# Performance work log

Hardware: AMD Instinct MI355X
Metric: run time of the kernel (lower is better)

The kernel has to match this reference:

```python
import jax, jax.numpy as jnp
import numpy as np

EPS = 1e-08


def setup_inputs() -> dict:
    key = jax.random.key(0)
    ks = jax.random.split(key, 9)
    B, T, H, W = 128, 32, 32, 32
    Z = 128
    d = {}
    d['x_seq'] = jax.random.normal(ks[0], (B, T, H, W), dtype=jnp.float32)
    # encoder MLP: 1024 -> 256 -> 128 (kaiming-ish scale)
    d['We1'] = jax.random.normal(ks[1], (H * W, 256), dtype=jnp.float32) * (2.0 / (H * W)) ** 0.5
    d['be1'] = jnp.zeros((256,), jnp.float32)
    d['We2'] = jax.random.normal(ks[2], (256, Z), dtype=jnp.float32) * (2.0 / 256) ** 0.5
    d['be2'] = jnp.zeros((Z,), jnp.float32)
    # context norm params
    d['gamma'] = jnp.ones((Z,), jnp.float32)
    d['beta'] = jnp.zeros((Z,), jnp.float32)
    # g_theta: (128+1)*2=258 -> 512 -> 256
    d['Wg1'] = jax.random.normal(ks[3], (258, 512), dtype=jnp.float32) * (2.0 / 258) ** 0.5
    d['bg1'] = jnp.zeros((512,), jnp.float32)
    d['Wg2'] = jax.random.normal(ks[4], (512, 256), dtype=jnp.float32) * (2.0 / 512) ** 0.5
    d['bg2'] = jnp.zeros((256,), jnp.float32)
    # f_phi: 256 -> 256 -> y_dim=4
    d['Wf'] = jax.random.normal(ks[5], (256, 256), dtype=jnp.float32) * (2.0 / 256) ** 0.5
    d['bf'] = jnp.zeros((256,), jnp.float32)
    d['Wy'] = jax.random.normal(ks[6], (256, 4), dtype=jnp.float32) * (1.0 / 256) ** 0.5
    d['by'] = jnp.zeros((4,), jnp.float32)
    return d


def reference(x_seq, We1, be1, We2, be2, gamma, beta, Wg1, bg1, Wg2, bg2, Wf, bf, Wy, by):
    B, T, H, W = x_seq.shape
    # Encoder (MLP stand-in), vectorized over the sequence dim
    x = x_seq.reshape(B, T, H * W)
    h = jax.nn.relu(jnp.einsum('btd,dk->btk', x, We1) + be1)
    z = jnp.einsum('btk,kz->btz', h, We2) + be2          # [B,T,128]
    # Context norm over the sequence dim (torch .var() is unbiased, ddof=1)
    mu = z.mean(axis=1, keepdims=True)
    sigma = jnp.sqrt(z.var(axis=1, keepdims=True, ddof=1) + EPS)
    z = (z - mu) / sigma * gamma + beta
    # Append temporal tag
    tag = jnp.broadcast_to(jnp.arange(T, dtype=z.dtype)[None, :, None], (B, T, 1))
    z = jnp.concatenate([z, tag], axis=2)                # [B,T,129]
    # Relation network over all T^2 ordered pairs, batched as one GEMM.
    # g_hidden = relu([z_i, z_j] @ Wg1 + bg1); split Wg1 to avoid materializing the concat.
    Wg1_a, Wg1_b = Wg1[:129], Wg1[129:]
    gi = jnp.einsum('bic,ch->bih', z, Wg1_a)             # [B,T,512]
    gj = jnp.einsum('bjc,ch->bjh', z, Wg1_b)             # [B,T,512]
    g_hidden = jax.nn.relu(gi[:, :, None, :] + gj[:, None, :, :] + bg1)  # [B,T,T,512]
    g_out = jax.nn.relu(jnp.einsum('bijh,hg->bijg', g_hidden, Wg2) + bg2)
    all_g = g_out.sum(axis=(1, 2))                       # [B,256]
    f_hidden = jax.nn.relu(all_g @ Wf + bf)
    y_pred_linear = f_hidden @ Wy + by                   # [B,4]
    y_pred = jnp.argmax(y_pred_linear, axis=1)
    return (y_pred_linear, y_pred)
```

## Files before the change

kernel.cpp:

```cpp
#include <hip/hip_runtime.h>
#include <hip/hip_bf16.h>

#define EPS 1e-8f

typedef __attribute__((ext_vector_type(8))) short short8;
typedef __attribute__((ext_vector_type(4))) float f32x4;

__device__ __forceinline__ unsigned short f2bf(float f) {
  union { float f; unsigned u; } v; v.f = f;
  unsigned r = v.u + 0x7fffu + ((v.u >> 16) & 1u);
  return (unsigned short)(r >> 16);
}
__device__ __forceinline__ float bf2f(unsigned short b) {
  union { unsigned u; float f; } v; v.u = ((unsigned)b) << 16;
  return v.f;
}
__device__ __forceinline__ unsigned pack_bf2(float lo, float hi) {
  unsigned r;
  asm("v_cvt_pk_bf16_f32 %0, %1, %2" : "=v"(r) : "v"(lo), "v"(hi));
  return r;
}

__global__ __launch_bounds__(256) void k0_prep(const float* __restrict__ We1,
                                               const float* __restrict__ We2,
                                               const float* __restrict__ Wg1,
                                               const float* __restrict__ Wg2,
                                               const float* __restrict__ Wf,
                                               unsigned short* __restrict__ We1T,
                                               unsigned short* __restrict__ We2T,
                                               unsigned short* __restrict__ Wg1T,
                                               unsigned short* __restrict__ Wg2T,
                                               unsigned short* __restrict__ WfT) {
  int idx = blockIdx.x * 256 + threadIdx.x;
  if (idx < 262144) {
    int n = idx >> 10, k = idx & 1023;
    We1T[idx] = f2bf(We1[k * 256 + n]);
  } else if (idx < 294912) {
    int e = idx - 262144;
    int n = e >> 8, k = e & 255;
    We2T[e] = f2bf(We2[k * 128 + n]);
  } else if (idx < 458752) {
    int e = idx - 294912;
    int n = e / 160, c = e % 160;
    float v = 0.f;
    if (c < 129) v = (n < 512) ? Wg1[c * 512 + n] : Wg1[(129 + c) * 512 + (n - 512)];
    Wg1T[e] = f2bf(v);
  } else if (idx < 589824) {
    int e = idx - 458752;
    int n = e >> 9, k = e & 511;
    Wg2T[e] = f2bf(Wg2[k * 256 + n]);
  } else {
    int e = idx - 589824;
    int n = e >> 8, k = e & 255;
    WfT[e] = f2bf(Wf[k * 256 + n]);
  }
}

__global__ __launch_bounds__(512, 2) void k1(const float* __restrict__ x,
                                             const unsigned short* __restrict__ We1T,
                                             const float* __restrict__ be1,
                                             unsigned short* __restrict__ h_bf) {
  __shared__ unsigned char As[2][8192];
  int tid = threadIdx.x, lane = tid & 63, w = tid >> 6;
  int m0 = blockIdx.x * 16;
  int srow = tid >> 5, skk = (tid & 31) * 8;
  int cb = w * 32;
  int row = lane & 15, kg = (lane >> 4) * 8;

  f32x4 acc[2] = {{0,0,0,0},{0,0,0,0}};

  auto stage = [&](int kc, int buf) {
    const float* src = x + (size_t)(m0 + srow) * 1024 + kc * 256 + skk;
    float4 a = *reinterpret_cast<const float4*>(src);
    float4 b = *reinterpret_cast<const float4*>(src + 4);
    uint4 pv;
    pv.x = pack_bf2(a.x, a.y); pv.y = pack_bf2(a.z, a.w);
    pv.z = pack_bf2(b.x, b.y); pv.w = pack_bf2(b.z, b.w);
    int addr = (srow * 512 + skk * 2) ^ ((srow & 7) << 4);
    *reinterpret_cast<uint4*>(&As[buf][addr]) = pv;
  };

  stage(0, 0);
  __syncthreads();
  for (int kc = 0; kc < 4; ++kc) {
    if (kc < 3) stage(kc + 1, (kc + 1) & 1);
    short8 breg[2][8];
#pragma unroll
    for (int cf = 0; cf < 2; ++cf)
#pragma unroll
      for (int ks = 0; ks < 8; ++ks)
        breg[cf][ks] = *reinterpret_cast<const short8*>(
            We1T + (size_t)(cb + cf * 16 + row) * 1024 + kc * 256 + ks * 32 + kg);
    const unsigned char* hc = &As[kc & 1][0];
#pragma unroll
    for (int ks = 0; ks < 8; ++ks) {
      int aoff = (row * 512 + ks * 64 + kg * 2) ^ ((row & 7) << 4);
      short8 af = *reinterpret_cast<const short8*>(hc + aoff);
      acc[0] = __builtin_amdgcn_mfma_f32_16x16x32_bf16(af, breg[0][ks], acc[0], 0, 0, 0);
      acc[1] = __builtin_amdgcn_mfma_f32_16x16x32_bf16(af, breg[1][ks], acc[1], 0, 0, 0);
    }
    __syncthreads();
  }
#pragma unroll
  for (int cf = 0; cf < 2; ++cf) {
    int col = cb + cf * 16 + row;
    float bias = be1[col];
#pragma unroll
    for (int r = 0; r < 4; ++r) {
      int orow = m0 + (lane >> 4) * 4 + r;
      h_bf[(size_t)orow * 256 + col] = f2bf(fmaxf(acc[cf][r] + bias, 0.f));
    }
  }
}

__global__ __launch_bounds__(256) void k2a(const unsigned short* __restrict__ h_bf,
                                           const unsigned short* __restrict__ We2T,
                                           const float* __restrict__ be2,
                                           const float* __restrict__ gamma,
                                           const float* __restrict__ beta,
                                           unsigned short* __restrict__ zc) {
  __shared__ unsigned char zcs[16384];
  __shared__ float zb[32][132];
  int b = blockIdx.x, tid = threadIdx.x, lane = tid & 63, w = tid >> 6;
  int row = lane & 15, kg = (lane >> 4) * 8;

  {
    int srow = tid >> 3, skk = (tid & 7) * 32;
#pragma unroll
    for (int q = 0; q < 4; ++q) {
      short8 v = *reinterpret_cast<const short8*>(
          h_bf + (size_t)(b * 32 + srow) * 256 + skk + q * 8);
      int addr = (srow * 512 + (skk + q * 8) * 2) ^ ((srow & 7) << 4);
      *reinterpret_cast<short8*>(&zcs[addr]) = v;
    }
  }
  short8 breg1[2][8];
#pragma unroll
  for (int cf = 0; cf < 2; ++cf)
#pragma unroll
    for (int ks = 0; ks < 8; ++ks)
      breg1[cf][ks] = *reinterpret_cast<const short8*>(
          We2T + (size_t)(w * 32 + cf * 16 + row) * 256 + ks * 32 + kg);
  __syncthreads();

  {
    f32x4 acc[2][2] = {{{0,0,0,0},{0,0,0,0}},{{0,0,0,0},{0,0,0,0}}};
#pragma unroll
    for (int ks = 0; ks < 8; ++ks) {
      int a0off = (row * 512 + ks * 64 + kg * 2) ^ ((row & 7) << 4);
      int a1off = ((16 + row) * 512 + ks * 64 + kg * 2) ^ ((row & 7) << 4);
      short8 a0 = *reinterpret_cast<const short8*>(&zcs[a0off]);
      short8 a1 = *reinterpret_cast<const short8*>(&zcs[a1off]);
#pragma unroll
      for (int cf = 0; cf < 2; ++cf) {
        acc[0][cf] = __builtin_amdgcn_mfma_f32_16x16x32_bf16(a0, breg1[cf][ks], acc[0][cf], 0, 0, 0);
        acc[1][cf] = __builtin_amdgcn_mfma_f32_16x16x32_bf16(a1, breg1[cf][ks], acc[1][cf], 0, 0, 0);
      }
    }
#pragma unroll
    for (int rf = 0; rf < 2; ++rf)
#pragma unroll
      for (int cf = 0; cf < 2; ++cf) {
        int col = w * 32 + cf * 16 + row;
        float bias = be2[col];
#pragma unroll
        for (int r = 0; r < 4; ++r)
          zb[rf * 16 + (lane >> 4) * 4 + r][col] = acc[rf][cf][r] + bias;
      }
  }
  __syncthreads();

  if (tid < 128) {
    float s = 0.f, s2 = 0.f;
#pragma unroll 4
    for (int t = 0; t < 32; ++t) { float v = zb[t][tid]; s += v; s2 += v * v; }
    float mu = s * (1.f / 32.f);
    float var = (s2 - 32.f * mu * mu) * (1.f / 31.f);
    float rs = 1.f / sqrtf(fmaxf(var, 0.f) + EPS);
    float g = gamma[tid], be = beta[tid];
#pragma unroll 4
    for (int t = 0; t < 32; ++t)
      zc[(size_t)(b * 32 + t) * 160 + tid] = f2bf((zb[t][tid] - mu) * rs * g + be);
  } else if (tid < 160) {
    for (int t = 0; t < 32; ++t)
      zc[(size_t)(b * 32 + t) * 160 + tid] = (tid == 128) ? f2bf((float)t) : 0;
  }
}

__global__ __launch_bounds__(512, 4) void k2b(const unsigned short* __restrict__ zc,
                                              const unsigned short* __restrict__ Wg1T,
                                              const float* __restrict__ bg1,
                                              unsigned short* __restrict__ g_all) {
  __shared__ unsigned char As[16384];
  int m0 = (blockIdx.x >> 2) * 32;
  int n0 = (blockIdx.x & 3) * 256;
  int tid = threadIdx.x, lane = tid & 63, w = tid >> 6;
  int row = lane & 15, kg = (lane >> 4) * 8;
  int c0 = n0 + w * 32;

  for (int ch = tid; ch < 640; ch += 512) {
    int r = ch / 20, c16 = ch % 20;
    short8 v = *reinterpret_cast<const short8*>(zc + (size_t)(m0 + r) * 160 + c16 * 8);
    int addr = (r * 512 + c16 * 16) ^ ((r & 7) << 4);
    *reinterpret_cast<short8*>(&As[addr]) = v;
  }
  short8 breg[2][5];
#pragma unroll
  for (int cf = 0; cf < 2; ++cf)
#pragma unroll
    for (int ks = 0; ks < 5; ++ks)
      breg[cf][ks] = *reinterpret_cast<const short8*>(
          Wg1T + (size_t)(c0 + cf * 16 + row) * 160 + ks * 32 + kg);
  __syncthreads();

  f32x4 acc[2][2] = {{{0,0,0,0},{0,0,0,0}},{{0,0,0,0},{0,0,0,0}}};
#pragma unroll
  for (int ks = 0; ks < 5; ++ks) {
    int a0off = (row * 512 + ks * 64 + kg * 2) ^ ((row & 7) << 4);
    int a1off = ((16 + row) * 512 + ks * 64 + kg * 2) ^ ((row & 7) << 4);
    short8 a0 = *reinterpret_cast<const short8*>(&As[a0off]);
    short8 a1 = *reinterpret_cast<const short8*>(&As[a1off]);
#pragma unroll
    for (int cf = 0; cf < 2; ++cf) {
      acc[0][cf] = __builtin_amdgcn_mfma_f32_16x16x32_bf16(a0, breg[cf][ks], acc[0][cf], 0, 0, 0);
      acc[1][cf] = __builtin_amdgcn_mfma_f32_16x16x32_bf16(a1, breg[cf][ks], acc[1][cf], 0, 0, 0);
    }
  }
#pragma unroll
  for (int cf = 0; cf < 2; ++cf) {
    int n = c0 + cf * 16 + row;
    float bias = (n < 512) ? bg1[n] : 0.f;
#pragma unroll
    for (int rf = 0; rf < 2; ++rf)
#pragma unroll
      for (int r = 0; r < 4; ++r) {
        int mrow = m0 + rf * 16 + (lane >> 4) * 4 + r;
        g_all[((size_t)mrow << 10) + n] = f2bf(acc[rf][cf][r] + bias);
      }
  }
}

__global__ __launch_bounds__(512, 2) void k3(const unsigned short* __restrict__ g_all,
                                             const unsigned short* __restrict__ Wg2T,
                                             const float* __restrict__ bg2,
                                             float* __restrict__ all_gp) {
  __shared__ unsigned char ldsH[2][32768];
  int b = blockIdx.x >> 1, hi = blockIdx.x & 1;
  int ii0 = hi * 16;
  int tid = threadIdx.x, lane = tid & 63, w = tid >> 6;
  int row = lane & 15, kg16 = (lane >> 4) * 16;
  int cb = w * 32;
  int p = tid >> 4, kslot = tid & 15;

  short8 breg[2][16];
#pragma unroll
  for (int cf = 0; cf < 2; ++cf)
#pragma unroll
    for (int ks = 0; ks < 16; ++ks)
      breg[cf][ks] = *reinterpret_cast<const short8*>(
          Wg2T + (size_t)(cb + cf * 16 + row) * 512 + ks * 32 + (lane >> 4) * 8);

  float gjf[32];
  {
    const unsigned short* gjp = g_all + ((size_t)(b * 32 + p) << 10) + 512 + kslot * 8;
#pragma unroll
    for (int q = 0; q < 4; ++q) {
      short8 gv = *reinterpret_cast<const short8*>(gjp + q * 128);
#pragma unroll
      for (int e = 0; e < 8; ++e) gjf[q * 8 + e] = bf2f((unsigned short)gv[e]);
    }
  }
  float biasv[2] = { bg2[cb + row], bg2[cb + 16 + row] };
  float accsum[2] = { 0.f, 0.f };

  short8 gv[4];
  auto hload = [&](int ii) {
    const unsigned short* gi = g_all + ((size_t)(b * 32 + ii) << 10) + kslot * 8;
#pragma unroll
    for (int q = 0; q < 4; ++q)
      gv[q] = *reinterpret_cast<const short8*>(gi + q * 128);
  };
  auto hstore = [&](int buf) {
    unsigned char* hb = &ldsH[buf][0] + p * 1024;
#pragma unroll
    for (int q = 0; q < 4; ++q) {
      uint4 pv;
      float f0 = fmaxf(bf2f((unsigned short)gv[q][0]) + gjf[q * 8 + 0], 0.f);
      float f1 = fmaxf(bf2f((unsigned short)gv[q][1]) + gjf[q * 8 + 1], 0.f);
      float f2 = fmaxf(bf2f((unsigned short)gv[q][2]) + gjf[q * 8 + 2], 0.f);
      float f3 = fmaxf(bf2f((unsigned short)gv[q][3]) + gjf[q * 8 + 3], 0.f);
      float f4 = fmaxf(bf2f((unsigned short)gv[q][4]) + gjf[q * 8 + 4], 0.f);
      float f5 = fmaxf(bf2f((unsigned short)gv[q][5]) + gjf[q * 8 + 5], 0.f);
      float f6 = fmaxf(bf2f((unsigned short)gv[q][6]) + gjf[q * 8 + 6], 0.f);
      float f7 = fmaxf(bf2f((unsigned short)gv[q][7]) + gjf[q * 8 + 7], 0.f);
      pv.x = pack_bf2(f0, f1); pv.y = pack_bf2(f2, f3);
      pv.z = pack_bf2(f4, f5); pv.w = pack_bf2(f6, f7);
      int addr = (kslot * 16 + q * 256) ^ ((p & 7) << 4);
      *reinterpret_cast<uint4*>(hb + addr) = pv;
    }
  };

  hload(ii0);
  hstore(0);
  __syncthreads();

  for (int it = 0; it < 16; ++it) {
    if (it < 15) hload(ii0 + it + 1);
    const unsigned char* hc = &ldsH[it & 1][0];
    f32x4 acc[2][2] = {{{0,0,0,0},{0,0,0,0}},{{0,0,0,0},{0,0,0,0}}};
    short8 a0 = *reinterpret_cast<const short8*>(hc + ((row * 1024 + kg16) ^ ((row & 7) << 4)));
    short8 a1 = *reinterpret_cast<const short8*>(hc + (((16 + row) * 1024 + kg16) ^ ((row & 7) << 4)));
#pragma unroll
    for (int ks = 0; ks < 16; ++ks) {
      short8 c0v = a0, c1v = a1;
      if (ks < 15) {
        a0 = *reinterpret_cast<const short8*>(hc + ((row * 1024 + (ks + 1) * 64 + kg16) ^ ((row & 7) << 4)));
        a1 = *reinterpret_cast<const short8*>(hc + (((16 + row) * 1024 + (ks + 1) * 64 + kg16) ^ ((row & 7) << 4)));
      }
      __builtin_amdgcn_s_setprio(1);
      acc[0][0] = __builtin_amdgcn_mfma_f32_16x16x32_bf16(c0v, breg[0][ks], acc[0][0], 0, 0, 0);
      acc[0][1] = __builtin_amdgcn_mfma_f32_16x16x32_bf16(c0v, breg[1][ks], acc[0][1], 0, 0, 0);
      acc[1][0] = __builtin_amdgcn_mfma_f32_16x16x32_bf16(c1v, breg[0][ks], acc[1][0], 0, 0, 0);
      acc[1][1] = __builtin_amdgcn_mfma_f32_16x16x32_bf16(c1v, breg[1][ks], acc[1][1], 0, 0, 0);
      __builtin_amdgcn_s_setprio(0);
    }
    if (it < 15) hstore((it + 1) & 1);
#pragma unroll
    for (int cf = 0; cf < 2; ++cf)
#pragma unroll
      for (int rf = 0; rf < 2; ++rf)
#pragma unroll
        for (int r = 0; r < 4; ++r)
          accsum[cf] += fmaxf(acc[rf][cf][r] + biasv[cf], 0.f);
    __syncthreads();
  }

#pragma unroll
  for (int cf = 0; cf < 2; ++cf) {
    accsum[cf] += __shfl_xor(accsum[cf], 16, 64);
    accsum[cf] += __shfl_xor(accsum[cf], 32, 64);
  }
  if ((lane >> 4) == 0) {
#pragma unroll
    for (int cf = 0; cf < 2; ++cf)
      all_gp[(size_t)(hi * 128 + b) * 256 + cb + cf * 16 + lane] = accsum[cf];
  }
}

__global__ __launch_bounds__(512) void k4(const float* __restrict__ all_gp,
                                          const unsigned short* __restrict__ WfT,
                                          const float* __restrict__ bfv,
                                          const float* __restrict__ Wy,
                                          const float* __restrict__ by,
                                          float* __restrict__ out) {
  __shared__ unsigned char As[8192];
  __shared__ float fh[16][264];
  __shared__ float wys[1024];
  __shared__ float yvs[16][4];
  int tid = threadIdx.x, lane = tid & 63, w = tid >> 6;
  int row = lane & 15, kg = (lane >> 4) * 8;
  int m0 = blockIdx.x * 16;

  {
    int r = tid >> 5, c8 = (tid & 31) * 8;
    const float* p0 = all_gp + (size_t)(m0 + r) * 256 + c8;
    const float* p1 = all_gp + (size_t)(128 + m0 + r) * 256 + c8;
    float4 a0 = *reinterpret_cast<const float4*>(p0);
    float4 a1 = *reinterpret_cast<const float4*>(p0 + 4);
    float4 b0 = *reinterpret_cast<const float4*>(p1);
    float4 b1 = *reinterpret_cast<const float4*>(p1 + 4);
    uint4 pv;
    pv.x = pack_bf2(a0.x + b0.x, a0.y + b0.y);
    pv.y = pack_bf2(a0.z + b0.z, a0.w + b0.w);
    pv.z = pack_bf2(a1.x + b1.x, a1.y + b1.y);
    pv.w = pack_bf2(a1.z + b1.z, a1.w + b1.w);
    int addr = (r * 512 + c8 * 2) ^ ((r & 7) << 4);
    *reinterpret_cast<uint4*>(&As[addr]) = pv;
  }
  wys[tid] = Wy[tid];
  wys[tid + 512] = Wy[tid + 512];
  short8 breg[2][8];
#pragma unroll
  for (int cf = 0; cf < 2; ++cf)
#pragma unroll
    for (int ks = 0; ks < 8; ++ks)
      breg[cf][ks] = *reinterpret_cast<const short8*>(
          WfT + (size_t)(w * 32 + cf * 16 + row) * 256 + ks * 32 + kg);
  __syncthreads();

  f32x4 acc[2] = {{0,0,0,0},{0,0,0,0}};
#pragma unroll
  for (int ks = 0; ks < 8; ++ks) {
    int aoff = (row * 512 + ks * 64 + kg * 2) ^ ((row & 7) << 4);
    short8 af = *reinterpret_cast<const short8*>(&As[aoff]);
    acc[0] = __builtin_amdgcn_mfma_f32_16x16x32_bf16(af, breg[0][ks], acc[0], 0, 0, 0);
    acc[1] = __builtin_amdgcn_mfma_f32_16x16x32_bf16(af, breg[1][ks], acc[1], 0, 0, 0);
  }
#pragma unroll
  for (int cf = 0; cf < 2; ++cf) {
    int col = w * 32 + cf * 16 + row;
    float bias = bfv[col];
#pragma unroll
    for (int r = 0; r < 4; ++r)
      fh[(lane >> 4) * 4 + r][col] = fmaxf(acc[cf][r] + bias, 0.f);
  }
  __syncthreads();

  if (tid < 64) {
    int r = tid >> 2, o = tid & 3;
    float y = by[o];
#pragma unroll 4
    for (int k = 0; k < 256; ++k) y += fh[r][k] * wys[k * 4 + o];
    yvs[r][o] = y;
    out[(m0 + r) * 4 + o] = y;
  }
  __syncthreads();
  if (tid < 16) {
    int am = 0;
    float best = yvs[tid][0];
#pragma unroll
    for (int o = 1; o < 4; ++o)
      if (yvs[tid][o] > best) { best = yvs[tid][o]; am = o; }
    out[512 + m0 + tid] = (float)am;
  }
}

extern "C" void kernel_launch(void* const* d_in, const int* in_sizes, int n_in,
                              void* d_out, int out_size, void* d_ws, size_t ws_size,
                              hipStream_t stream) {
  const float* x     = (const float*)d_in[0];
  const float* We1   = (const float*)d_in[1];
  const float* be1   = (const float*)d_in[2];
  const float* We2   = (const float*)d_in[3];
  const float* be2   = (const float*)d_in[4];
  const float* gamma = (const float*)d_in[5];
  const float* beta  = (const float*)d_in[6];
  const float* Wg1   = (const float*)d_in[7];
  const float* bg1   = (const float*)d_in[8];
  const float* Wg2   = (const float*)d_in[9];
  const float* bg2   = (const float*)d_in[10];
  const float* Wf    = (const float*)d_in[11];
  const float* bff   = (const float*)d_in[12];
  const float* Wy    = (const float*)d_in[13];
  const float* by    = (const float*)d_in[14];

  char* ws = (char*)d_ws;
  unsigned short* h_bf  = (unsigned short*)(ws + 0);
  unsigned short* g_all = (unsigned short*)(ws + 2097152);
  unsigned short* We1T  = (unsigned short*)(ws + 10485760);
  unsigned short* We2T  = (unsigned short*)(ws + 11010048);
  unsigned short* Wg1T  = (unsigned short*)(ws + 11075584);
  unsigned short* Wg2T  = (unsigned short*)(ws + 11403264);
  float*          all_gp= (float*)(ws + 11665408);
  unsigned short* WfT   = (unsigned short*)(ws + 11927552);
  unsigned short* zc    = (unsigned short*)(ws + 12058624);
  float*          out   = (float*)d_out;

  k0_prep<<<2560, 256, 0, stream>>>(We1, We2, Wg1, Wg2, Wf, We1T, We2T, Wg1T, Wg2T, WfT);
  k1<<<256, 512, 0, stream>>>(x, We1T, be1, h_bf);
  k2a<<<128, 256, 0, stream>>>(h_bf, We2T, be2, gamma, beta, zc);
  k2b<<<512, 512, 0, stream>>>(zc, Wg1T, bg1, g_all);
  k3<<<256, 512, 0, stream>>>(g_all, Wg2T, bg2, all_gp);
  k4<<<8, 512, 0, stream>>>(all_gp, WfT, bff, Wy, by, out);
}
```

Before: 84.02 us.

## Fuse context-norm with Wg1 projection and switch pair GEMM to 32x32 MFMA

Merges k2a and k2b into a single kernel. The normalized z tile stays in shared memory and is multiplied directly by Wg1, which drops the zc round trip through global memory and one launch. The cost is that each of the four column-quarter blocks per batch recomputes the We2 projection and the normalization. Separately, k3's pair GEMM now uses 32x32x16 bf16 MFMA with one 16-float accumulator per wave instead of four 16x16x32 tiles, which changes the register and LDS read pattern.

```diff
diff --git a/kernel.cpp b/kernel.cpp
--- a/kernel.cpp
+++ b/kernel.cpp
@@ -5,6 +5,7 @@
 
 typedef __attribute__((ext_vector_type(8))) short short8;
 typedef __attribute__((ext_vector_type(4))) float f32x4;
+typedef __attribute__((ext_vector_type(16))) float f32x16;
 
 __device__ __forceinline__ unsigned short f2bf(float f) {
   union { float f; unsigned u; } v; v.f = f;
@@ -113,15 +114,18 @@
   }
 }
 
-__global__ __launch_bounds__(256) void k2a(const unsigned short* __restrict__ h_bf,
-                                           const unsigned short* __restrict__ We2T,
-                                           const float* __restrict__ be2,
-                                           const float* __restrict__ gamma,
-                                           const float* __restrict__ beta,
-                                           unsigned short* __restrict__ zc) {
+__global__ __launch_bounds__(256) void k2(const unsigned short* __restrict__ h_bf,
+                                          const unsigned short* __restrict__ We2T,
+                                          const float* __restrict__ be2,
+                                          const float* __restrict__ gamma,
+                                          const float* __restrict__ beta,
+                                          const unsigned short* __restrict__ Wg1T,
+                                          const float* __restrict__ bg1,
+                                          unsigned short* __restrict__ g_all) {
   __shared__ unsigned char zcs[16384];
   __shared__ float zb[32][132];
-  int b = blockIdx.x, tid = threadIdx.x, lane = tid & 63, w = tid >> 6;
+  int b = blockIdx.x >> 2, nq = blockIdx.x & 3;
+  int tid = threadIdx.x, lane = tid & 63, w = tid >> 6;
   int row = lane & 15, kg = (lane >> 4) * 8;
 
   {
@@ -179,64 +183,58 @@
     float rs = 1.f / sqrtf(fmaxf(var, 0.f) + EPS);
     float g = gamma[tid], be = beta[tid];
 #pragma unroll 4
-    for (int t = 0; t < 32; ++t)
-      zc[(size_t)(b * 32 + t) * 160 + tid] = f2bf((zb[t][tid] - mu) * rs * g + be);
+    for (int t = 0; t < 32; ++t) {
+      unsigned short v = f2bf((zb[t][tid] - mu) * rs * g + be);
+      int addr = (t * 512 + tid * 2) ^ ((t & 7) << 4);
+      *reinterpret_cast<unsigned short*>(&zcs[addr]) = v;
+    }
   } else if (tid < 160) {
-    for (int t = 0; t < 32; ++t)
-      zc[(size_t)(b * 32 + t) * 160 + tid] = (tid == 128) ? f2bf((float)t) : 0;
-  }
-}
-
-__global__ __launch_bounds__(512, 4) void k2b(const unsigned short* __restrict__ zc,
-                                              const unsigned short* __restrict__ Wg1T,
-                                              const float* __restrict__ bg1,
-                                              unsigned short* __restrict__ g_all) {
-  __shared__ unsigned char As[16384];
-  int m0 = (blockIdx.x >> 2) * 32;
-  int n0 = (blockIdx.x & 3) * 256;
-  int tid = threadIdx.x, lane = tid & 63, w = tid >> 6;
-  int row = lane & 15, kg = (lane >> 4) * 8;
-  int c0 = n0 + w * 32;
-
-  for (int ch = tid; ch < 640; ch += 512) {
-    int r = ch / 20, c16 = ch % 20;
-    short8 v = *reinterpret_cast<const short8*>(zc + (size_t)(m0 + r) * 160 + c16 * 8);
-    int addr = (r * 512 + c16 * 16) ^ ((r & 7) << 4);
-    *reinterpret_cast<short8*>(&As[addr]) = v;
-  }
-  short8 breg[2][5];
-#pragma unroll
-  for (int cf = 0; cf < 2; ++cf)
+    for (int t = 0; t < 32; ++t) {
+      unsigned short v = (tid == 128) ? f2bf((float)t) : 0;
+      int addr = (t * 512 + tid * 2) ^ ((t & 7) << 4);
+      *reinterpret_cast<unsigned short*>(&zcs[addr]) = v;
+    }
+  }
+  __syncthreads();
+
+  {
+    int n0 = nq * 256 + w * 64;
+    short8 af[2][5];
+#pragma unroll
+    for (int rf = 0; rf < 2; ++rf)
+#pragma unroll
+      for (int ks = 0; ks < 5; ++ks) {
+        int aoff = ((rf * 16 + row) * 512 + ks * 64 + kg * 2) ^ ((row & 7) << 4);
+        af[rf][ks] = *reinterpret_cast<const short8*>(&zcs[aoff]);
+      }
+    short8 breg[4][5];
+#pragma unroll
+    for (int cf = 0; cf < 4; ++cf)
+#pragma unroll
+      for (int ks = 0; ks < 5; ++ks)
+        breg[cf][ks] = *reinterpret_cast<const short8*>(
+            Wg1T + (size_t)(n0 + cf * 16 + row) * 160 + ks * 32 + kg);
+    f32x4 acc[2][4] = {{{0,0,0,0},{0,0,0,0},{0,0,0,0},{0,0,0,0}},
+                       {{0,0,0,0},{0,0,0,0},{0,0,0,0},{0,0,0,0}}};
 #pragma unroll
     for (int ks = 0; ks < 5; ++ks)
-      breg[cf][ks] = *reinterpret_cast<const short8*>(
-          Wg1T + (size_t)(c0 + cf * 16 + row) * 160 + ks * 32 + kg);
-  __syncthreads();
-
-  f32x4 acc[2][2] = {{{0,0,0,0},{0,0,0,0}},{{0,0,0,0},{0,0,0,0}}};
-#pragma unroll
-  for (int ks = 0; ks < 5; ++ks) {
-    int a0off = (row * 512 + ks * 64 + kg * 2) ^ ((row & 7) << 4);
-    int a1off = ((16 + row) * 512 + ks * 64 + kg * 2) ^ ((row & 7) << 4);
-    short8 a0 = *reinterpret_cast<const short8*>(&As[a0off]);
-    short8 a1 = *reinterpret_cast<const short8*>(&As[a1off]);
-#pragma unroll
-    for (int cf = 0; cf < 2; ++cf) {
-      acc[0][cf] = __builtin_amdgcn_mfma_f32_16x16x32_bf16(a0, breg[cf][ks], acc[0][cf], 0, 0, 0);
-      acc[1][cf] = __builtin_amdgcn_mfma_f32_16x16x32_bf16(a1, breg[cf][ks], acc[1][cf], 0, 0, 0);
-    }
-  }
-#pragma unroll
-  for (int cf = 0; cf < 2; ++cf) {
-    int n = c0 + cf * 16 + row;
-    float bias = (n < 512) ? bg1[n] : 0.f;
-#pragma unroll
-    for (int rf = 0; rf < 2; ++rf)
-#pragma unroll
-      for (int r = 0; r < 4; ++r) {
-        int mrow = m0 + rf * 16 + (lane >> 4) * 4 + r;
-        g_all[((size_t)mrow << 10) + n] = f2bf(acc[rf][cf][r] + bias);
+#pragma unroll
+      for (int cf = 0; cf < 4; ++cf) {
+        acc[0][cf] = __builtin_amdgcn_mfma_f32_16x16x32_bf16(af[0][ks], breg[cf][ks], acc[0][cf], 0, 0, 0);
+        acc[1][cf] = __builtin_amdgcn_mfma_f32_16x16x32_bf16(af[1][ks], breg[cf][ks], acc[1][cf], 0, 0, 0);
       }
+#pragma unroll
+    for (int cf = 0; cf < 4; ++cf) {
+      int n = n0 + cf * 16 + row;
+      float bias = (n < 512) ? bg1[n] : 0.f;
+#pragma unroll
+      for (int rf = 0; rf < 2; ++rf)
+#pragma unroll
+        for (int r = 0; r < 4; ++r) {
+          int t = rf * 16 + (lane >> 4) * 4 + r;
+          g_all[((size_t)(b * 32 + t) << 10) + n] = f2bf(acc[rf][cf][r] + bias);
+        }
+    }
   }
 }
 
@@ -248,30 +246,28 @@
   int b = blockIdx.x >> 1, hi = blockIdx.x & 1;
   int ii0 = hi * 16;
   int tid = threadIdx.x, lane = tid & 63, w = tid >> 6;
-  int row = lane & 15, kg16 = (lane >> 4) * 16;
+  int l31 = lane & 31, lhi = lane >> 5;
   int cb = w * 32;
   int p = tid >> 4, kslot = tid & 15;
 
-  short8 breg[2][16];
-#pragma unroll
-  for (int cf = 0; cf < 2; ++cf)
-#pragma unroll
-    for (int ks = 0; ks < 16; ++ks)
-      breg[cf][ks] = *reinterpret_cast<const short8*>(
-          Wg2T + (size_t)(cb + cf * 16 + row) * 512 + ks * 32 + (lane >> 4) * 8);
+  short8 breg[32];
+#pragma unroll
+  for (int s = 0; s < 32; ++s)
+    breg[s] = *reinterpret_cast<const short8*>(
+        Wg2T + (size_t)(cb + l31) * 512 + s * 16 + lhi * 8);
 
   float gjf[32];
   {
     const unsigned short* gjp = g_all + ((size_t)(b * 32 + p) << 10) + 512 + kslot * 8;
 #pragma unroll
     for (int q = 0; q < 4; ++q) {
-      short8 gv = *reinterpret_cast<const short8*>(gjp + q * 128);
-#pragma unroll
-      for (int e = 0; e < 8; ++e) gjf[q * 8 + e] = bf2f((unsigned short)gv[e]);
-    }
-  }
-  float biasv[2] = { bg2[cb + row], bg2[cb + 16 + row] };
-  float accsum[2] = { 0.f, 0.f };
+      short8 gv0 = *reinterpret_cast<const short8*>(gjp + q * 128);
+#pragma unroll
+      for (int e = 0; e < 8; ++e) gjf[q * 8 + e] = bf2f((unsigned short)gv0[e]);
+    }
+  }
+  float bias = bg2[cb + l31];
+  float accsum = 0.f;
 
   short8 gv[4];
   auto hload = [&](int ii) {
@@ -307,44 +303,32 @@
   for (int it = 0; it < 16; ++it) {
     if (it < 15) hload(ii0 + it + 1);
     const unsigned char* hc = &ldsH[it & 1][0];
-    f32x4 acc[2][2] = {{{0,0,0,0},{0,0,0,0}},{{0,0,0,0},{0,0,0,0}}};
-    short8 a0 = *reinterpret_cast<const short8*>(hc + ((row * 1024 + kg16) ^ ((row & 7) << 4)));
-    short8 a1 = *reinterpret_cast<const short8*>(hc + (((16 + row) * 1024 + kg16) ^ ((row & 7) << 4)));
-#pragma unroll
-    for (int ks = 0; ks < 16; ++ks) {
-      short8 c0v = a0, c1v = a1;
-      if (ks < 15) {
-        a0 = *reinterpret_cast<const short8*>(hc + ((row * 1024 + (ks + 1) * 64 + kg16) ^ ((row & 7) << 4)));
-        a1 = *reinterpret_cast<const short8*>(hc + (((16 + row) * 1024 + (ks + 1) * 64 + kg16) ^ ((row & 7) << 4)));
-      }
+    f32x16 acc = {0.f,0.f,0.f,0.f,0.f,0.f,0.f,0.f,0.f,0.f,0.f,0.f,0.f,0.f,0.f,0.f};
+    short8 ar[4];
+#pragma unroll
+    for (int s = 0; s < 4; ++s)
+      ar[s] = *reinterpret_cast<const short8*>(
+          hc + ((l31 * 1024 + s * 32 + lhi * 16) ^ ((l31 & 7) << 4)));
+#pragma unroll
+    for (int s = 0; s < 32; ++s) {
+      short8 cur = ar[s & 3];
+      if (s < 28)
+        ar[s & 3] = *reinterpret_cast<const short8*>(
+            hc + ((l31 * 1024 + (s + 4) * 32 + lhi * 16) ^ ((l31 & 7) << 4)));
       __builtin_amdgcn_s_setprio(1);
-      acc[0][0] = __builtin_amdgcn_mfma_f32_16x16x32_bf16(c0v, breg[0][ks], acc[0][0], 0, 0, 0);
-      acc[0][1] = __builtin_amdgcn_mfma_f32_16x16x32_bf16(c0v, breg[1][ks], acc[0][1], 0, 0, 0);
-      acc[1][0] = __builtin_amdgcn_mfma_f32_16x16x32_bf16(c1v, breg[0][ks], acc[1][0], 0, 0, 0);
-      acc[1][1] = __builtin_amdgcn_mfma_f32_16x16x32_bf16(c1v, breg[1][ks], acc[1][1], 0, 0, 0);
+      acc = __builtin_amdgcn_mfma_f32_32x32x16_bf16(cur, breg[s], acc, 0, 0, 0);
       __builtin_amdgcn_s_setprio(0);
     }
     if (it < 15) hstore((it + 1) & 1);
 #pragma unroll
-    for (int cf = 0; cf < 2; ++cf)
-#pragma unroll
-      for (int rf = 0; rf < 2; ++rf)
-#pragma unroll
-        for (int r = 0; r < 4; ++r)
-          accsum[cf] += fmaxf(acc[rf][cf][r] + biasv[cf], 0.f);
+    for (int r = 0; r < 16; ++r)
+      accsum += fmaxf(acc[r] + bias, 0.f);
     __syncthreads();
   }
 
-#pragma unroll
-  for (int cf = 0; cf < 2; ++cf) {
-    accsum[cf] += __shfl_xor(accsum[cf], 16, 64);
-    accsum[cf] += __shfl_xor(accsum[cf], 32, 64);
-  }
-  if ((lane >> 4) == 0) {
-#pragma unroll
-    for (int cf = 0; cf < 2; ++cf)
-      all_gp[(size_t)(hi * 128 + b) * 256 + cb + cf * 16 + lane] = accsum[cf];
-  }
+  accsum += __shfl_xor(accsum, 32, 64);
+  if (lane < 32)
+    all_gp[(size_t)(hi * 128 + b) * 256 + cb + l31] = accsum;
 }
 
 __global__ __launch_bounds__(512) void k4(const float* __restrict__ all_gp,
@@ -453,13 +437,11 @@
   unsigned short* Wg2T  = (unsigned short*)(ws + 11403264);
   float*          all_gp= (float*)(ws + 11665408);
   unsigned short* WfT   = (unsigned short*)(ws + 11927552);
-  unsigned short* zc    = (unsigned short*)(ws + 12058624);
   float*          out   = (float*)d_out;
 
   k0_prep<<<2560, 256, 0, stream>>>(We1, We2, Wg1, Wg2, Wf, We1T, We2T, Wg1T, Wg2T, WfT);
   k1<<<256, 512, 0, stream>>>(x, We1T, be1, h_bf);
-  k2a<<<128, 256, 0, stream>>>(h_bf, We2T, be2, gamma, beta, zc);
-  k2b<<<512, 512, 0, stream>>>(zc, Wg1T, bg1, g_all);
+  k2<<<512, 256, 0, stream>>>(h_bf, We2T, be2, gamma, beta, Wg1T, bg1, g_all);
   k3<<<256, 512, 0, stream>>>(g_all, Wg2T, bg2, all_gp);
   k4<<<8, 512, 0, stream>>>(all_gp, WfT, bff, Wy, by, out);
 }
```

After: 88.62 us. +5.5%, slower.

## Fuse encoder GEMMs with context norm and tile weight transposes through LDS

Applied to the files above, without the earlier changes.

Merges the first encoder GEMM (k1) with the second GEMM and context-norm kernel (k2a) into one per-batch kernel, k1f. The ReLU hidden activations stay in LDS instead of round-tripping through global memory, and one launch goes away. The weight-prep kernel now transposes 32x32 tiles through shared memory, so both global reads and writes are coalesced instead of strided. The cost is that the fused GEMM runs on 128 blocks instead of 256, which lowers parallelism on the first GEMM. Waves 4-7 also compute unused columns in the second GEMM: their We2T reads fall past the end of the We2T buffer and the results are discarded by the col<128 guard.

```diff
diff --git a/kernel.cpp b/kernel.cpp
--- a/kernel.cpp
+++ b/kernel.cpp
@@ -31,109 +31,143 @@
                                                unsigned short* __restrict__ Wg1T,
                                                unsigned short* __restrict__ Wg2T,
                                                unsigned short* __restrict__ WfT) {
-  int idx = blockIdx.x * 256 + threadIdx.x;
-  if (idx < 262144) {
-    int n = idx >> 10, k = idx & 1023;
-    We1T[idx] = f2bf(We1[k * 256 + n]);
-  } else if (idx < 294912) {
-    int e = idx - 262144;
-    int n = e >> 8, k = e & 255;
-    We2T[e] = f2bf(We2[k * 128 + n]);
-  } else if (idx < 458752) {
-    int e = idx - 294912;
-    int n = e / 160, c = e % 160;
-    float v = 0.f;
-    if (c < 129) v = (n < 512) ? Wg1[c * 512 + n] : Wg1[(129 + c) * 512 + (n - 512)];
-    Wg1T[e] = f2bf(v);
-  } else if (idx < 589824) {
-    int e = idx - 458752;
-    int n = e >> 9, k = e & 511;
-    Wg2T[e] = f2bf(Wg2[k * 256 + n]);
+  __shared__ float ld[32][33];
+  int t = blockIdx.x, tid = threadIdx.x;
+  int r0 = tid >> 5, c = tid & 31;
+
+  if (t < 256) {
+    int rb = (t >> 3) * 32, cb = (t & 7) * 32;
+#pragma unroll
+    for (int j = 0; j < 4; ++j)
+      ld[r0 + j * 8][c] = We1[(size_t)(rb + r0 + j * 8) * 256 + cb + c];
+    __syncthreads();
+#pragma unroll
+    for (int j = 0; j < 4; ++j)
+      We1T[(size_t)(cb + r0 + j * 8) * 1024 + rb + c] = f2bf(ld[c][r0 + j * 8]);
+  } else if (t < 288) {
+    int u = t - 256;
+    int rb = (u >> 2) * 32, cb = (u & 3) * 32;
+#pragma unroll
+    for (int j = 0; j < 4; ++j)
+      ld[r0 + j * 8][c] = We2[(size_t)(rb + r0 + j * 8) * 128 + cb + c];
+    __syncthreads();
+#pragma unroll
+    for (int j = 0; j < 4; ++j)
+      We2T[(size_t)(cb + r0 + j * 8) * 256 + rb + c] = f2bf(ld[c][r0 + j * 8]);
+  } else if (t < 416) {
+    int u = t - 288;
+    int rb = (u >> 3) * 32, cb = (u & 7) * 32;
+#pragma unroll
+    for (int j = 0; j < 4; ++j)
+      ld[r0 + j * 8][c] = Wg2[(size_t)(rb + r0 + j * 8) * 256 + cb + c];
+    __syncthreads();
+#pragma unroll
+    for (int j = 0; j < 4; ++j)
+      Wg2T[(size_t)(cb + r0 + j * 8) * 512 + rb + c] = f2bf(ld[c][r0 + j * 8]);
+  } else if (t < 480) {
+    int u = t - 416;
+    int rb = (u >> 3) * 32, cb = (u & 7) * 32;
+#pragma unroll
+    for (int j = 0; j < 4; ++j)
+      ld[r0 + j * 8][c] = Wf[(size_t)(rb + r0 + j * 8) * 256 + cb + c];
+    __syncthreads();
+#pragma unroll
+    for (int j = 0; j < 4; ++j)
+      WfT[(size_t)(cb + r0 + j * 8) * 256 + rb + c] = f2bf(ld[c][r0 + j * 8]);
   } else {
-    int e = idx - 589824;
-    int n = e >> 8, k = e & 255;
-    WfT[e] = f2bf(Wf[k * 256 + n]);
-  }
-}
-
-__global__ __launch_bounds__(512, 2) void k1(const float* __restrict__ x,
-                                             const unsigned short* __restrict__ We1T,
-                                             const float* __restrict__ be1,
-                                             unsigned short* __restrict__ h_bf) {
-  __shared__ unsigned char As[2][8192];
-  int tid = threadIdx.x, lane = tid & 63, w = tid >> 6;
-  int m0 = blockIdx.x * 16;
-  int srow = tid >> 5, skk = (tid & 31) * 8;
-  int cb = w * 32;
-  int row = lane & 15, kg = (lane >> 4) * 8;
-
-  f32x4 acc[2] = {{0,0,0,0},{0,0,0,0}};
-
-  auto stage = [&](int kc, int buf) {
-    const float* src = x + (size_t)(m0 + srow) * 1024 + kc * 256 + skk;
-    float4 a = *reinterpret_cast<const float4*>(src);
-    float4 b = *reinterpret_cast<const float4*>(src + 4);
-    uint4 pv;
-    pv.x = pack_bf2(a.x, a.y); pv.y = pack_bf2(a.z, a.w);
-    pv.z = pack_bf2(b.x, b.y); pv.w = pack_bf2(b.z, b.w);
-    int addr = (srow * 512 + skk * 2) ^ ((srow & 7) << 4);
-    *reinterpret_cast<uint4*>(&As[buf][addr]) = pv;
-  };
-
-  stage(0, 0);
-  __syncthreads();
-  for (int kc = 0; kc < 4; ++kc) {
-    if (kc < 3) stage(kc + 1, (kc + 1) & 1);
-    short8 breg[2][8];
-#pragma unroll
-    for (int cf = 0; cf < 2; ++cf)
-#pragma unroll
-      for (int ks = 0; ks < 8; ++ks)
-        breg[cf][ks] = *reinterpret_cast<const short8*>(
-            We1T + (size_t)(cb + cf * 16 + row) * 1024 + kc * 256 + ks * 32 + kg);
-    const unsigned char* hc = &As[kc & 1][0];
-#pragma unroll
-    for (int ks = 0; ks < 8; ++ks) {
-      int aoff = (row * 512 + ks * 64 + kg * 2) ^ ((row & 7) << 4);
-      short8 af = *reinterpret_cast<const short8*>(hc + aoff);
-      acc[0] = __builtin_amdgcn_mfma_f32_16x16x32_bf16(af, breg[0][ks], acc[0], 0, 0, 0);
-      acc[1] = __builtin_amdgcn_mfma_f32_16x16x32_bf16(af, breg[1][ks], acc[1], 0, 0, 0);
-    }
-    __syncthreads();
-  }
-#pragma unroll
-  for (int cf = 0; cf < 2; ++cf) {
-    int col = cb + cf * 16 + row;
-    float bias = be1[col];
-#pragma unroll
-    for (int r = 0; r < 4; ++r) {
-      int orow = m0 + (lane >> 4) * 4 + r;
-      h_bf[(size_t)orow * 256 + col] = f2bf(fmaxf(acc[cf][r] + bias, 0.f));
-    }
-  }
-}
-
-__global__ __launch_bounds__(256) void k2a(const unsigned short* __restrict__ h_bf,
+    int u = t - 480;
+    int nb = (u / 5) * 32, cb5 = (u % 5) * 32;
+#pragma unroll
+    for (int j = 0; j < 4; ++j) {
+      int cloc = r0 + j * 8, cidx = cb5 + cloc, n = nb + c;
+      float v = 0.f;
+      if (cidx < 129)
+        v = (n < 512) ? Wg1[(size_t)cidx * 512 + n]
+                      : Wg1[(size_t)(129 + cidx) * 512 + (n - 512)];
+      ld[cloc][c] = v;
+    }
+    __syncthreads();
+#pragma unroll
+    for (int j = 0; j < 4; ++j)
+      Wg1T[(size_t)(nb + r0 + j * 8) * 160 + cb5 + c] = f2bf(ld[c][r0 + j * 8]);
+  }
+}
+
+__global__ __launch_bounds__(512) void k1f(const float* __restrict__ x,
+                                           const unsigned short* __restrict__ We1T,
+                                           const float* __restrict__ be1,
                                            const unsigned short* __restrict__ We2T,
                                            const float* __restrict__ be2,
                                            const float* __restrict__ gamma,
                                            const float* __restrict__ beta,
                                            unsigned short* __restrict__ zc) {
-  __shared__ unsigned char zcs[16384];
+  __shared__ unsigned char As[2][16384];
   __shared__ float zb[32][132];
   int b = blockIdx.x, tid = threadIdx.x, lane = tid & 63, w = tid >> 6;
   int row = lane & 15, kg = (lane >> 4) * 8;
-
-  {
-    int srow = tid >> 3, skk = (tid & 7) * 32;
-#pragma unroll
-    for (int q = 0; q < 4; ++q) {
-      short8 v = *reinterpret_cast<const short8*>(
-          h_bf + (size_t)(b * 32 + srow) * 256 + skk + q * 8);
-      int addr = (srow * 512 + (skk + q * 8) * 2) ^ ((srow & 7) << 4);
-      *reinterpret_cast<short8*>(&zcs[addr]) = v;
-    }
-  }
+  int cb = w * 32;
+  int srow = tid >> 4, sc16 = (tid & 15) * 16;
+
+  auto stage = [&](int kc, int buf) {
+    const float* src = x + (size_t)(b * 32 + srow) * 1024 + kc * 256 + sc16;
+    float4 a  = reinterpret_cast<const float4*>(src)[0];
+    float4 bb = reinterpret_cast<const float4*>(src)[1];
+    float4 cc = reinterpret_cast<const float4*>(src)[2];
+    float4 dd = reinterpret_cast<const float4*>(src)[3];
+    uint4 p0, p1;
+    p0.x = pack_bf2(a.x, a.y);  p0.y = pack_bf2(a.z, a.w);
+    p0.z = pack_bf2(bb.x, bb.y); p0.w = pack_bf2(bb.z, bb.w);
+    p1.x = pack_bf2(cc.x, cc.y); p1.y = pack_bf2(cc.z, cc.w);
+    p1.z = pack_bf2(dd.x, dd.y); p1.w = pack_bf2(dd.z, dd.w);
+    int base = srow * 512 + sc16 * 2, swz = (srow & 7) << 4;
+    *reinterpret_cast<uint4*>(&As[buf][base ^ swz]) = p0;
+    *reinterpret_cast<uint4*>(&As[buf][(base + 16) ^ swz]) = p1;
+  };
+
+  f32x4 acc1[2][2] = {{{0,0,0,0},{0,0,0,0}},{{0,0,0,0},{0,0,0,0}}};
+  stage(0, 0);
+  __syncthreads();
+  for (int kc = 0; kc < 4; ++kc) {
+    if (kc < 3) stage(kc + 1, (kc + 1) & 1);
+    short8 breg[2][8];
+#pragma unroll
+    for (int cf = 0; cf < 2; ++cf)
+#pragma unroll
+      for (int ks = 0; ks < 8; ++ks)
+        breg[cf][ks] = *reinterpret_cast<const short8*>(
+            We1T + (size_t)(cb + cf * 16 + row) * 1024 + kc * 256 + ks * 32 + kg);
+    const unsigned char* hc = &As[kc & 1][0];
+#pragma unroll
+    for (int ks = 0; ks < 8; ++ks) {
+      int a0off = (row * 512 + ks * 64 + kg * 2) ^ ((row & 7) << 4);
+      int a1off = ((16 + row) * 512 + ks * 64 + kg * 2) ^ ((row & 7) << 4);
+      short8 a0 = *reinterpret_cast<const short8*>(hc + a0off);
+      short8 a1 = *reinterpret_cast<const short8*>(hc + a1off);
+#pragma unroll
+      for (int cf = 0; cf < 2; ++cf) {
+        acc1[0][cf] = __builtin_amdgcn_mfma_f32_16x16x32_bf16(a0, breg[cf][ks], acc1[0][cf], 0, 0, 0);
+        acc1[1][cf] = __builtin_amdgcn_mfma_f32_16x16x32_bf16(a1, breg[cf][ks], acc1[1][cf], 0, 0, 0);
+      }
+    }
+    __syncthreads();
+  }
+
+#pragma unroll
+  for (int cf = 0; cf < 2; ++cf) {
+    int col = cb + cf * 16 + row;
+    float bias = be1[col];
+#pragma unroll
+    for (int rf = 0; rf < 2; ++rf)
+#pragma unroll
+      for (int r = 0; r < 4; ++r) {
+        int rr = rf * 16 + (lane >> 4) * 4 + r;
+        unsigned short hv = f2bf(fmaxf(acc1[rf][cf][r] + bias, 0.f));
+        int addr = (rr * 512 + col * 2) ^ ((rr & 7) << 4);
+        *reinterpret_cast<unsigned short*>(&As[0][addr]) = hv;
+      }
+  }
+  __syncthreads();
+
   short8 breg1[2][8];
 #pragma unroll
   for (int cf = 0; cf < 2; ++cf)
@@ -141,16 +175,15 @@
     for (int ks = 0; ks < 8; ++ks)
       breg1[cf][ks] = *reinterpret_cast<const short8*>(
           We2T + (size_t)(w * 32 + cf * 16 + row) * 256 + ks * 32 + kg);
-  __syncthreads();
-
   {
     f32x4 acc[2][2] = {{{0,0,0,0},{0,0,0,0}},{{0,0,0,0},{0,0,0,0}}};
+    const unsigned char* hc = &As[0][0];
 #pragma unroll
     for (int ks = 0; ks < 8; ++ks) {
       int a0off = (row * 512 + ks * 64 + kg * 2) ^ ((row & 7) << 4);
       int a1off = ((16 + row) * 512 + ks * 64 + kg * 2) ^ ((row & 7) << 4);
-      short8 a0 = *reinterpret_cast<const short8*>(&zcs[a0off]);
-      short8 a1 = *reinterpret_cast<const short8*>(&zcs[a1off]);
+      short8 a0 = *reinterpret_cast<const short8*>(hc + a0off);
+      short8 a1 = *reinterpret_cast<const short8*>(hc + a1off);
 #pragma unroll
       for (int cf = 0; cf < 2; ++cf) {
         acc[0][cf] = __builtin_amdgcn_mfma_f32_16x16x32_bf16(a0, breg1[cf][ks], acc[0][cf], 0, 0, 0);
@@ -162,10 +195,12 @@
 #pragma unroll
       for (int cf = 0; cf < 2; ++cf) {
         int col = w * 32 + cf * 16 + row;
-        float bias = be2[col];
-#pragma unroll
-        for (int r = 0; r < 4; ++r)
-          zb[rf * 16 + (lane >> 4) * 4 + r][col] = acc[rf][cf][r] + bias;
+        if (col < 128) {
+          float bias = be2[col];
+#pragma unroll
+          for (int r = 0; r < 4; ++r)
+            zb[rf * 16 + (lane >> 4) * 4 + r][col] = acc[rf][cf][r] + bias;
+        }
       }
   }
   __syncthreads();
@@ -187,6 +222,7 @@
   }
 }
 
+
 __global__ __launch_bounds__(512, 4) void k2b(const unsigned short* __restrict__ zc,
                                               const unsigned short* __restrict__ Wg1T,
                                               const float* __restrict__ bg1,
@@ -248,7 +284,7 @@
   int b = blockIdx.x >> 1, hi = blockIdx.x & 1;
   int ii0 = hi * 16;
   int tid = threadIdx.x, lane = tid & 63, w = tid >> 6;
-  int row = lane & 15, kg16 = (lane >> 4) * 16;
+  int row = lane & 15, kg = (lane >> 4) * 8;
   int cb = w * 32;
   int p = tid >> 4, kslot = tid & 15;
 
@@ -258,16 +294,16 @@
 #pragma unroll
     for (int ks = 0; ks < 16; ++ks)
       breg[cf][ks] = *reinterpret_cast<const short8*>(
-          Wg2T + (size_t)(cb + cf * 16 + row) * 512 + ks * 32 + (lane >> 4) * 8);
+          Wg2T + (size_t)(cb + cf * 16 + row) * 512 + ks * 32 + kg);
 
   float gjf[32];
   {
     const unsigned short* gjp = g_all + ((size_t)(b * 32 + p) << 10) + 512 + kslot * 8;
 #pragma unroll
     for (int q = 0; q < 4; ++q) {
-      short8 gv = *reinterpret_cast<const short8*>(gjp + q * 128);
-#pragma unroll
-      for (int e = 0; e < 8; ++e) gjf[q * 8 + e] = bf2f((unsigned short)gv[e]);
+      short8 gv0 = *reinterpret_cast<const short8*>(gjp + q * 128);
+#pragma unroll
+      for (int e = 0; e < 8; ++e) gjf[q * 8 + e] = bf2f((unsigned short)gv0[e]);
     }
   }
   float biasv[2] = { bg2[cb + row], bg2[cb + 16 + row] };
@@ -308,14 +344,14 @@
     if (it < 15) hload(ii0 + it + 1);
     const unsigned char* hc = &ldsH[it & 1][0];
     f32x4 acc[2][2] = {{{0,0,0,0},{0,0,0,0}},{{0,0,0,0},{0,0,0,0}}};
-    short8 a0 = *reinterpret_cast<const short8*>(hc + ((row * 1024 + kg16) ^ ((row & 7) << 4)));
-    short8 a1 = *reinterpret_cast<const short8*>(hc + (((16 + row) * 1024 + kg16) ^ ((row & 7) << 4)));
+    short8 a0 = *reinterpret_cast<const short8*>(hc + ((row * 1024 + kg * 2) ^ ((row & 7) << 4)));
+    short8 a1 = *reinterpret_cast<const short8*>(hc + (((16 + row) * 1024 + kg * 2) ^ ((row & 7) << 4)));
 #pragma unroll
     for (int ks = 0; ks < 16; ++ks) {
       short8 c0v = a0, c1v = a1;
       if (ks < 15) {
-        a0 = *reinterpret_cast<const short8*>(hc + ((row * 1024 + (ks + 1) * 64 + kg16) ^ ((row & 7) << 4)));
-        a1 = *reinterpret_cast<const short8*>(hc + (((16 + row) * 1024 + (ks + 1) * 64 + kg16) ^ ((row & 7) << 4)));
+        a0 = *reinterpret_cast<const short8*>(hc + ((row * 1024 + (ks + 1) * 64 + kg * 2) ^ ((row & 7) << 4)));
+        a1 = *reinterpret_cast<const short8*>(hc + (((16 + row) * 1024 + (ks + 1) * 64 + kg * 2) ^ ((row & 7) << 4)));
       }
       __builtin_amdgcn_s_setprio(1);
       acc[0][0] = __builtin_amdgcn_mfma_f32_16x16x32_bf16(c0v, breg[0][ks], acc[0][0], 0, 0, 0);
@@ -363,17 +399,20 @@
 
   {
     int r = tid >> 5, c8 = (tid & 31) * 8;
-    const float* p0 = all_gp + (size_t)(m0 + r) * 256 + c8;
-    const float* p1 = all_gp + (size_t)(128 + m0 + r) * 256 + c8;
-    float4 a0 = *reinterpret_cast<const float4*>(p0);
-    float4 a1 = *reinterpret_cast<const float4*>(p0 + 4);
-    float4 b0 = *reinterpret_cast<const float4*>(p1);
-    float4 b1 = *reinterpret_cast<const float4*>(p1 + 4);
+    float s[8];
+#pragma unroll
+    for (int e = 0; e < 8; ++e) s[e] = 0.f;
+#pragma unroll
+    for (int q = 0; q < 2; ++q) {
+      const float* p0 = all_gp + (size_t)(q * 128 + m0 + r) * 256 + c8;
+      float4 a0 = *reinterpret_cast<const float4*>(p0);
+      float4 a1 = *reinterpret_cast<const float4*>(p0 + 4);
+      s[0] += a0.x; s[1] += a0.y; s[2] += a0.z; s[3] += a0.w;
+      s[4] += a1.x; s[5] += a1.y; s[6] += a1.z; s[7] += a1.w;
+    }
     uint4 pv;
-    pv.x = pack_bf2(a0.x + b0.x, a0.y + b0.y);
-    pv.y = pack_bf2(a0.z + b0.z, a0.w + b0.w);
-    pv.z = pack_bf2(a1.x + b1.x, a1.y + b1.y);
-    pv.w = pack_bf2(a1.z + b1.z, a1.w + b1.w);
+    pv.x = pack_bf2(s[0], s[1]); pv.y = pack_bf2(s[2], s[3]);
+    pv.z = pack_bf2(s[4], s[5]); pv.w = pack_bf2(s[6], s[7]);
     int addr = (r * 512 + c8 * 2) ^ ((r & 7) << 4);
     *reinterpret_cast<uint4*>(&As[addr]) = pv;
   }
@@ -445,20 +484,18 @@
   const float* by    = (const float*)d_in[14];
 
   char* ws = (char*)d_ws;
-  unsigned short* h_bf  = (unsigned short*)(ws + 0);
-  unsigned short* g_all = (unsigned short*)(ws + 2097152);
-  unsigned short* We1T  = (unsigned short*)(ws + 10485760);
-  unsigned short* We2T  = (unsigned short*)(ws + 11010048);
-  unsigned short* Wg1T  = (unsigned short*)(ws + 11075584);
-  unsigned short* Wg2T  = (unsigned short*)(ws + 11403264);
-  float*          all_gp= (float*)(ws + 11665408);
-  unsigned short* WfT   = (unsigned short*)(ws + 11927552);
-  unsigned short* zc    = (unsigned short*)(ws + 12058624);
+  unsigned short* g_all = (unsigned short*)(ws + 0);
+  unsigned short* We1T  = (unsigned short*)(ws + 8388608);
+  unsigned short* We2T  = (unsigned short*)(ws + 8912896);
+  unsigned short* Wg1T  = (unsigned short*)(ws + 9175040);
+  unsigned short* Wg2T  = (unsigned short*)(ws + 9502720);
+  unsigned short* WfT   = (unsigned short*)(ws + 9764864);
+  float*          all_gp= (float*)(ws + 9895936);
+  unsigned short* zc    = (unsigned short*)(ws + 10158080);
   float*          out   = (float*)d_out;
 
-  k0_prep<<<2560, 256, 0, stream>>>(We1, We2, Wg1, Wg2, Wf, We1T, We2T, Wg1T, Wg2T, WfT);
-  k1<<<256, 512, 0, stream>>>(x, We1T, be1, h_bf);
-  k2a<<<128, 256, 0, stream>>>(h_bf, We2T, be2, gamma, beta, zc);
+  k0_prep<<<640, 256, 0, stream>>>(We1, We2, Wg1, Wg2, Wf, We1T, We2T, Wg1T, Wg2T, WfT);
+  k1f<<<128, 512, 0, stream>>>(x, We1T, be1, We2T, be2, gamma, beta, zc);
   k2b<<<512, 512, 0, stream>>>(zc, Wg1T, bg1, g_all);
   k3<<<256, 512, 0, stream>>>(g_all, Wg2T, bg2, all_gp);
   k4<<<8, 512, 0, stream>>>(all_gp, WfT, bff, Wy, by, out);
```

Result: slower. 85.96 us (+2.3%).
